# Kernel tuning notes

Hardware: AMD Instinct MI355X
Metric: run time of the kernel (lower is better)

Reference implementation:

```python
import jax, jax.numpy as jnp
import numpy as np

B, L, H = 2, 512, 128

def setup_inputs() -> dict:
    key = jax.random.key(0)
    k1, k2, k3, _ = jax.random.split(key, 4)
    x = jax.random.normal(k1, (B, L, H), jnp.float32)
    y = jax.random.normal(k2, (B, L, H), jnp.float32)
    W_weight = jax.random.normal(k3, (H, 3 * H), jnp.float32) / np.sqrt(3 * H).astype(np.float32)
    W_bias = jnp.zeros((H,), jnp.float32)
    return {"x": x, "y": y, "W_weight": W_weight, "W_bias": W_bias}

def _span_max_context(x):
    """context[b,i,j,h] = max_{k=min(i,j)..max(i,j)} x[b,k,h], shape [B,L,L,H].
    Equivalent to the torch loop of diagonal running-max + symmetric scatter."""
    Bb, Ll, Hh = x.shape
    neg = jnp.full((Bb, 1, Hh), -jnp.inf, x.dtype)
    x_pad = jnp.concatenate([x, neg], axis=1)              # [B,L+1,H]
    d = jnp.arange(Ll)[:, None]                            # diagonal offset
    j = jnp.arange(Ll)[None, :]                            # start position
    shift_idx = jnp.minimum(d + j, Ll)                     # [L,L]; L -> -inf pad
    X2 = x_pad[:, shift_idx, :]                            # X2[b,d,j] = x[b,j+d]
    D = jax.lax.cummax(X2, axis=1)                         # D[b,d,j] = max_{k=j..j+d} x[b,k]
    i = jnp.arange(Ll)[:, None]
    jj = jnp.arange(Ll)[None, :]
    off = jnp.abs(i - jj)                                  # |i-j|
    lo = jnp.minimum(i, jj)                                # min(i,j)
    return D[:, off, lo, :]                                # [B,L,L,H]

def reference(x, y, W_weight, W_bias):
    Hh = x.shape[-1]
    ctx = _span_max_context(x)
    # Split W over the concat [x_i, y_j, context_ij] to avoid a [B,L,L,3H] intermediate.
    Wx, Wy, Wc = W_weight[:, :Hh], W_weight[:, Hh:2 * Hh], W_weight[:, 2 * Hh:]
    t = (jnp.einsum('blh,gh->blg', x, Wx)[:, :, None, :]
         + jnp.einsum('blh,gh->blg', y, Wy)[:, None, :, :]
         + jnp.einsum('bijh,gh->bijg', ctx, Wc)
         + W_bias)
    return jax.nn.gelu(t, approximate=False)               # [B,L,L,H]
```

## Files before the change

kernel.cpp:

```cpp
#include <hip/hip_runtime.h>
#include <hip/hip_bf16.h>

#define LL 512
#define HH 128
#define NBATCH 2
#define NT 32
#define NPAIR (NT*(NT+1)/2)

typedef float f32x4 __attribute__((ext_vector_type(4)));
typedef short s16x8 __attribute__((ext_vector_type(8)));
typedef short s16x4 __attribute__((ext_vector_type(4)));

__device__ __forceinline__ unsigned short f2bfu(float f){
  __hip_bfloat16 h = __float2bfloat16(f);
  return __builtin_bit_cast(unsigned short, h);
}
__device__ __forceinline__ short f2bf(float f){
  __hip_bfloat16 h = __float2bfloat16(f);
  return __builtin_bit_cast(short, h);
}
__device__ __forceinline__ f32x4 max4v(f32x4 a, f32x4 b){
  f32x4 r; r[0]=fmaxf(a[0],b[0]); r[1]=fmaxf(a[1],b[1]);
  r[2]=fmaxf(a[2],b[2]); r[3]=fmaxf(a[3],b[3]); return r;
}
__device__ __forceinline__ float gelu_f(float v){
  float inner = v * fmaf(0.044715f, v*v, 1.0f);
  float e = __expf(1.5957691216f * inner);
  float s = __fdividef(1.0f, e + 1.0f);
  return fmaf(-v, s, v);
}
__device__ __forceinline__ f32x4 gelu4(f32x4 v){
  f32x4 r;
  #pragma unroll
  for (int i=0;i<4;++i) r[i] = gelu_f(v[i]);
  return r;
}

__global__ void prep_kernel(const float* __restrict__ x, const float* __restrict__ y,
                            const float* __restrict__ W, const float* __restrict__ bias,
                            float* __restrict__ t1, float* __restrict__ t2){
  int l = blockIdx.x, b = blockIdx.y;
  __shared__ float xs[HH], ys[HH];
  int tid = threadIdx.x;
  size_t base = ((size_t)b*LL + l)*HH;
  xs[tid] = x[base + tid];
  ys[tid] = y[base + tid];
  __syncthreads();
  const float4* wr1 = (const float4*)(W + (size_t)tid*384);
  const float4* wr2 = (const float4*)(W + (size_t)tid*384 + 128);
  const float4* xs4 = (const float4*)xs;
  const float4* ys4 = (const float4*)ys;
  float s1 = 0.f, s2 = 0.f;
  #pragma unroll
  for (int q=0;q<32;++q){
    float4 a = xs4[q], w = wr1[q];
    s1 = fmaf(a.x,w.x, fmaf(a.y,w.y, fmaf(a.z,w.z, fmaf(a.w,w.w, s1))));
    float4 c = ys4[q], w2 = wr2[q];
    s2 = fmaf(c.x,w2.x, fmaf(c.y,w2.y, fmaf(c.z,w2.z, fmaf(c.w,w2.w, s2))));
  }
  t1[base + tid] = s1 + bias[tid];
  t2[base + tid] = s2;
}

__global__ void misc_kernel(const float* __restrict__ x, const float* __restrict__ W,
                            float* __restrict__ bmax, short* __restrict__ Wcb){
  int blk = blockIdx.x, tid = threadIdx.x;
  if (blk < NBATCH*NT){
    int b = blk >> 5, t = blk & 31;
    float m = -INFINITY;
    #pragma unroll
    for (int r=0;r<16;++r) m = fmaxf(m, x[((size_t)b*LL + t*16 + r)*HH + tid]);
    bmax[(size_t)blk*HH + tid] = m;
  } else {
    int g = blk - NBATCH*NT;
    Wcb[g*HH + tid] = f2bf(W[(size_t)g*384 + 256 + tid]);
  }
}

__global__ __launch_bounds__(512, 4) void ctx_kernel(
    const float* __restrict__ x, const float* __restrict__ t1,
    const float* __restrict__ t2, const float* __restrict__ bmax,
    const short* __restrict__ Wcb, float* __restrict__ out)
{
  __shared__ unsigned short sfxS[16][HH];
  __shared__ unsigned short pfxS[16][HH];
  __shared__ float gmaxS[HH];
  __shared__ unsigned short Atile[256*HH];

  const int tid = threadIdx.x;
  const int b = blockIdx.y;
  int ti = 0, tj;
  { int rem = blockIdx.x;
    while (rem >= NT - ti){ rem -= NT - ti; ++ti; }
    tj = ti + rem; }

  if (ti != tj && tid < 3*HH) {
    int role = tid >> 7;
    int h = tid & (HH-1);
    if (role == 0){
      const float* xp = x + ((size_t)b*LL + ti*16)*HH + h;
      float v[16];
      #pragma unroll
      for (int r=0;r<16;++r) v[r] = xp[(size_t)r*HH];
      float run = -INFINITY;
      #pragma unroll
      for (int r=15;r>=0;--r){ run = fmaxf(run, v[r]); sfxS[r][h] = f2bfu(run); }
    } else if (role == 1){
      const float* xp = x + ((size_t)b*LL + tj*16)*HH + h;
      float v[16];
      #pragma unroll
      for (int r=0;r<16;++r) v[r] = xp[(size_t)r*HH];
      float run = -INFINITY;
      #pragma unroll
      for (int r=0;r<16;++r){ run = fmaxf(run, v[r]); pfxS[r][h] = f2bfu(run); }
    } else {
      float g = -INFINITY;
      for (int t = ti+1; t < tj; ++t)
        g = fmaxf(g, bmax[((size_t)b*NT + t)*HH + h]);
      gmaxS[h] = g;
    }
  }
  __syncthreads();

  {
    const int grp = tid >> 5;
    const int hq  = (tid & 31) * 4;
    auto storeA = [&](int p, f32x4 v){
      int e = p*HH + (hq ^ ((p&7)<<3));
      s16x4 sv = { f2bf(v[0]), f2bf(v[1]), f2bf(v[2]), f2bf(v[3]) };
      *(s16x4*)&Atile[e] = sv;
    };
    auto unpk4 = [&](const unsigned short* pp)->f32x4{
      uint2 u = *(const uint2*)pp;
      f32x4 r;
      r[0] = __uint_as_float(u.x << 16);
      r[1] = __uint_as_float(u.x & 0xFFFF0000u);
      r[2] = __uint_as_float(u.y << 16);
      r[3] = __uint_as_float(u.y & 0xFFFF0000u);
      return r;
    };
    if (ti != tj){
      f32x4 fx = *(const f32x4*)&gmaxS[hq];
      fx = max4v(fx, unpk4(&sfxS[grp][hq]));
      #pragma unroll
      for (int q=0;q<16;++q){
        f32x4 v = max4v(fx, unpk4(&pfxS[q][hq]));
        storeA(grp*16 + q, v);
      }
    } else {
      const float* xbase = x + ((size_t)b*LL + ti*16)*HH + hq;
      f32x4 base = *(const f32x4*)(xbase + (size_t)grp*HH);
      storeA(grp*16 + grp, base);
      f32x4 cur = base;
      for (int q=grp+1;q<16;++q){
        cur = max4v(cur, *(const f32x4*)(xbase + (size_t)q*HH));
        storeA(grp*16 + q, cur);
      }
      cur = base;
      for (int q=grp-1;q>=0;--q){
        cur = max4v(cur, *(const f32x4*)(xbase + (size_t)q*HH));
        storeA(grp*16 + q, cur);
      }
    }
  }
  __syncthreads();

  const int w   = tid >> 6;
  const int l   = tid & 63;
  const int l16 = l & 15, lhi = l >> 4;

  s16x8 wcf[4];
  #pragma unroll
  for (int kb=0;kb<4;++kb)
    wcf[kb] = *(const s16x8*)(Wcb + (size_t)(w*16 + l16)*HH + kb*32 + lhi*8);

  const int g0 = w*16 + lhi*4;
  const int swz = (l16 & 7) << 3;
  const int qrow = tj*16 + l16;
  const size_t t_qoff = ((size_t)b*LL + qrow)*HH + g0;
  const bool offd = (ti != tj);

  #pragma unroll
  for (int pt=0; pt<16; ++pt){
    const int p = pt*16 + l16;
    f32x4 acc = (f32x4){0.f,0.f,0.f,0.f};
    #pragma unroll
    for (int kb=0;kb<4;++kb){
      int hh2 = (kb*32 + lhi*8) ^ swz;
      s16x8 bf8 = *(const s16x8*)&Atile[p*HH + hh2];
      acc = __builtin_amdgcn_mfma_f32_16x16x32_bf16(wcf[kb], bf8, acc, 0, 0, 0);
    }
    const int irow = ti*16 + pt;
    const size_t t_ioff = ((size_t)b*LL + irow)*HH + g0;
    f32x4 t1i = *(const f32x4*)(t1 + t_ioff);
    f32x4 t2j = *(const f32x4*)(t2 + t_qoff);
    f32x4 o1 = gelu4(acc + t1i + t2j);
    *(f32x4*)(out + ((size_t)(b*LL + irow)*LL + qrow)*HH + g0) = o1;
    if (offd){
      f32x4 t1j = *(const f32x4*)(t1 + t_qoff);
      f32x4 t2i = *(const f32x4*)(t2 + t_ioff);
      f32x4 o2 = gelu4(acc + t1j + t2i);
      *(f32x4*)(out + ((size_t)(b*LL + qrow)*LL + irow)*HH + g0) = o2;
    }
  }
}

extern "C" void kernel_launch(void* const* d_in, const int* in_sizes, int n_in,
                              void* d_out, int out_size, void* d_ws, size_t ws_size,
                              hipStream_t stream) {
  const float* x    = (const float*)d_in[0];
  const float* y    = (const float*)d_in[1];
  const float* W    = (const float*)d_in[2];
  const float* bias = (const float*)d_in[3];
  float* out = (float*)d_out;

  float* t1 = (float*)d_ws;
  float* t2 = t1 + (size_t)NBATCH*LL*HH;
  float* bmax = t2 + (size_t)NBATCH*LL*HH;
  short* Wcb = (short*)(bmax + (size_t)NBATCH*NT*HH);

  prep_kernel<<<dim3(LL, NBATCH), HH, 0, stream>>>(x, y, W, bias, t1, t2);
  misc_kernel<<<NBATCH*NT + HH, HH, 0, stream>>>(x, W, bmax, Wcb);
  ctx_kernel<<<dim3(NPAIR, NBATCH), 512, 0, stream>>>(x, t1, t2, bmax, Wcb, out);
}
```

Measured before the change: 98.88 us.

## Build context operand in registers and sparse-table diagonal tiles, merge prep kernels

Folds the misc kernel into the prep kernel, so there is one fewer launch. The off-diagonal path no longer materializes a 64KB LDS A-tile. It folds the global max into the prefix values held in registers, then forms each MFMA operand by taking a packed bf16 max against swizzled suffix rows, which cuts LDS use and raises occupancy. Diagonal tiles now build a log-step sparse table in LDS instead of serial per-thread scans, and the global-max reduction is split over two thread groups. The risks are extra ALU work on packed bf16 and a difference in rounding: prefix and suffix are each rounded to bf16 before the max.

```diff
diff --git a/kernel.cpp b/kernel.cpp
--- a/kernel.cpp
+++ b/kernel.cpp
@@ -5,23 +5,28 @@
 #define HH 128
 #define NBATCH 2
 #define NT 32
-#define NPAIR (NT*(NT+1)/2)
+#define NOFF (NT*(NT-1)/2)
 
 typedef float f32x4 __attribute__((ext_vector_type(4)));
 typedef short s16x8 __attribute__((ext_vector_type(8)));
-typedef short s16x4 __attribute__((ext_vector_type(4)));
+typedef unsigned int u32x4 __attribute__((ext_vector_type(4)));
 
 __device__ __forceinline__ unsigned short f2bfu(float f){
   __hip_bfloat16 h = __float2bfloat16(f);
   return __builtin_bit_cast(unsigned short, h);
 }
-__device__ __forceinline__ short f2bf(float f){
-  __hip_bfloat16 h = __float2bfloat16(f);
-  return __builtin_bit_cast(short, h);
-}
-__device__ __forceinline__ f32x4 max4v(f32x4 a, f32x4 b){
-  f32x4 r; r[0]=fmaxf(a[0],b[0]); r[1]=fmaxf(a[1],b[1]);
-  r[2]=fmaxf(a[2],b[2]); r[3]=fmaxf(a[3],b[3]); return r;
+__device__ __forceinline__ unsigned int bmax2(unsigned int a, unsigned int b){
+  float lo = fmaxf(__uint_as_float(a << 16), __uint_as_float(b << 16));
+  float hi = fmaxf(__uint_as_float(a & 0xFFFF0000u), __uint_as_float(b & 0xFFFF0000u));
+  return __float_as_uint(hi) | (__float_as_uint(lo) >> 16);
+}
+__device__ __forceinline__ unsigned int fold3(unsigned int p, float gl, float gh,
+                                              float g2l, float g2h){
+  float lo = fmaxf(fmaxf(__uint_as_float(p << 16), gl), g2l);
+  float hi = fmaxf(fmaxf(__uint_as_float(p & 0xFFFF0000u), gh), g2h);
+  unsigned int lor = (__float_as_uint(lo) + 0x8000u) >> 16;
+  unsigned int hir = (__float_as_uint(hi) + 0x8000u) & 0xFFFF0000u;
+  return hir | lor;
 }
 __device__ __forceinline__ float gelu_f(float v){
   float inner = v * fmaf(0.044715f, v*v, 1.0f);
@@ -38,42 +43,40 @@
 
 __global__ void prep_kernel(const float* __restrict__ x, const float* __restrict__ y,
                             const float* __restrict__ W, const float* __restrict__ bias,
-                            float* __restrict__ t1, float* __restrict__ t2){
-  int l = blockIdx.x, b = blockIdx.y;
-  __shared__ float xs[HH], ys[HH];
-  int tid = threadIdx.x;
-  size_t base = ((size_t)b*LL + l)*HH;
-  xs[tid] = x[base + tid];
-  ys[tid] = y[base + tid];
-  __syncthreads();
-  const float4* wr1 = (const float4*)(W + (size_t)tid*384);
-  const float4* wr2 = (const float4*)(W + (size_t)tid*384 + 128);
-  const float4* xs4 = (const float4*)xs;
-  const float4* ys4 = (const float4*)ys;
-  float s1 = 0.f, s2 = 0.f;
-  #pragma unroll
-  for (int q=0;q<32;++q){
-    float4 a = xs4[q], w = wr1[q];
-    s1 = fmaf(a.x,w.x, fmaf(a.y,w.y, fmaf(a.z,w.z, fmaf(a.w,w.w, s1))));
-    float4 c = ys4[q], w2 = wr2[q];
-    s2 = fmaf(c.x,w2.x, fmaf(c.y,w2.y, fmaf(c.z,w2.z, fmaf(c.w,w2.w, s2))));
-  }
-  t1[base + tid] = s1 + bias[tid];
-  t2[base + tid] = s2;
-}
-
-__global__ void misc_kernel(const float* __restrict__ x, const float* __restrict__ W,
+                            float* __restrict__ t1, float* __restrict__ t2,
                             float* __restrict__ bmax, short* __restrict__ Wcb){
   int blk = blockIdx.x, tid = threadIdx.x;
-  if (blk < NBATCH*NT){
-    int b = blk >> 5, t = blk & 31;
+  if (blk < NBATCH*LL){
+    int b = blk >> 9, l = blk & (LL-1);
+    __shared__ float xs[HH], ys[HH];
+    size_t base = ((size_t)b*LL + l)*HH;
+    xs[tid] = x[base + tid];
+    ys[tid] = y[base + tid];
+    __syncthreads();
+    const float4* wr1 = (const float4*)(W + (size_t)tid*384);
+    const float4* wr2 = (const float4*)(W + (size_t)tid*384 + 128);
+    const float4* xs4 = (const float4*)xs;
+    const float4* ys4 = (const float4*)ys;
+    float s1 = 0.f, s2 = 0.f;
+    #pragma unroll
+    for (int q=0;q<32;++q){
+      float4 a = xs4[q], w = wr1[q];
+      s1 = fmaf(a.x,w.x, fmaf(a.y,w.y, fmaf(a.z,w.z, fmaf(a.w,w.w, s1))));
+      float4 c = ys4[q], w2 = wr2[q];
+      s2 = fmaf(c.x,w2.x, fmaf(c.y,w2.y, fmaf(c.z,w2.z, fmaf(c.w,w2.w, s2))));
+    }
+    t1[base + tid] = s1 + bias[tid];
+    t2[base + tid] = s2;
+  } else if (blk < NBATCH*LL + NBATCH*NT){
+    int e = blk - NBATCH*LL;
+    int b = e >> 5, t = e & 31;
     float m = -INFINITY;
     #pragma unroll
     for (int r=0;r<16;++r) m = fmaxf(m, x[((size_t)b*LL + t*16 + r)*HH + tid]);
-    bmax[(size_t)blk*HH + tid] = m;
+    bmax[(size_t)e*HH + tid] = m;
   } else {
-    int g = blk - NBATCH*NT;
-    Wcb[g*HH + tid] = f2bf(W[(size_t)g*384 + 256 + tid]);
+    int g = blk - (NBATCH*LL + NBATCH*NT);
+    Wcb[g*HH + tid] = (short)f2bfu(W[(size_t)g*384 + 256 + tid]);
   }
 }
 
@@ -82,125 +85,161 @@
     const float* __restrict__ t2, const float* __restrict__ bmax,
     const short* __restrict__ Wcb, float* __restrict__ out)
 {
-  __shared__ unsigned short sfxS[16][HH];
-  __shared__ unsigned short pfxS[16][HH];
-  __shared__ float gmaxS[HH];
-  __shared__ unsigned short Atile[256*HH];
-
+  __shared__ __align__(16) unsigned int shbuf[5*16*64];
   const int tid = threadIdx.x;
   const int b = blockIdx.y;
-  int ti = 0, tj;
-  { int rem = blockIdx.x;
-    while (rem >= NT - ti){ rem -= NT - ti; ++ti; }
-    tj = ti + rem; }
-
-  if (ti != tj && tid < 3*HH) {
-    int role = tid >> 7;
-    int h = tid & (HH-1);
-    if (role == 0){
-      const float* xp = x + ((size_t)b*LL + ti*16)*HH + h;
-      float v[16];
-      #pragma unroll
-      for (int r=0;r<16;++r) v[r] = xp[(size_t)r*HH];
-      float run = -INFINITY;
-      #pragma unroll
-      for (int r=15;r>=0;--r){ run = fmaxf(run, v[r]); sfxS[r][h] = f2bfu(run); }
-    } else if (role == 1){
-      const float* xp = x + ((size_t)b*LL + tj*16)*HH + h;
-      float v[16];
-      #pragma unroll
-      for (int r=0;r<16;++r) v[r] = xp[(size_t)r*HH];
-      float run = -INFINITY;
-      #pragma unroll
-      for (int r=0;r<16;++r){ run = fmaxf(run, v[r]); pfxS[r][h] = f2bfu(run); }
-    } else {
-      float g = -INFINITY;
-      for (int t = ti+1; t < tj; ++t)
-        g = fmaxf(g, bmax[((size_t)b*NT + t)*HH + h]);
-      gmaxS[h] = g;
-    }
-  }
-  __syncthreads();
-
-  {
-    const int grp = tid >> 5;
-    const int hq  = (tid & 31) * 4;
-    auto storeA = [&](int p, f32x4 v){
-      int e = p*HH + (hq ^ ((p&7)<<3));
-      s16x4 sv = { f2bf(v[0]), f2bf(v[1]), f2bf(v[2]), f2bf(v[3]) };
-      *(s16x4*)&Atile[e] = sv;
-    };
-    auto unpk4 = [&](const unsigned short* pp)->f32x4{
-      uint2 u = *(const uint2*)pp;
-      f32x4 r;
-      r[0] = __uint_as_float(u.x << 16);
-      r[1] = __uint_as_float(u.x & 0xFFFF0000u);
-      r[2] = __uint_as_float(u.y << 16);
-      r[3] = __uint_as_float(u.y & 0xFFFF0000u);
-      return r;
-    };
-    if (ti != tj){
-      f32x4 fx = *(const f32x4*)&gmaxS[hq];
-      fx = max4v(fx, unpk4(&sfxS[grp][hq]));
-      #pragma unroll
-      for (int q=0;q<16;++q){
-        f32x4 v = max4v(fx, unpk4(&pfxS[q][hq]));
-        storeA(grp*16 + q, v);
-      }
-    } else {
-      const float* xbase = x + ((size_t)b*LL + ti*16)*HH + hq;
-      f32x4 base = *(const f32x4*)(xbase + (size_t)grp*HH);
-      storeA(grp*16 + grp, base);
-      f32x4 cur = base;
-      for (int q=grp+1;q<16;++q){
-        cur = max4v(cur, *(const f32x4*)(xbase + (size_t)q*HH));
-        storeA(grp*16 + q, cur);
-      }
-      cur = base;
-      for (int q=grp-1;q>=0;--q){
-        cur = max4v(cur, *(const f32x4*)(xbase + (size_t)q*HH));
-        storeA(grp*16 + q, cur);
-      }
-    }
-  }
-  __syncthreads();
-
-  const int w   = tid >> 6;
-  const int l   = tid & 63;
-  const int l16 = l & 15, lhi = l >> 4;
+  const int w = tid >> 6, l = tid & 63, l16 = l & 15, lhi = l >> 4;
+  const int g0 = w*16 + lhi*4;
 
   s16x8 wcf[4];
   #pragma unroll
   for (int kb=0;kb<4;++kb)
     wcf[kb] = *(const s16x8*)(Wcb + (size_t)(w*16 + l16)*HH + kb*32 + lhi*8);
 
-  const int g0 = w*16 + lhi*4;
-  const int swz = (l16 & 7) << 3;
-  const int qrow = tj*16 + l16;
-  const size_t t_qoff = ((size_t)b*LL + qrow)*HH + g0;
-  const bool offd = (ti != tj);
-
-  #pragma unroll
-  for (int pt=0; pt<16; ++pt){
-    const int p = pt*16 + l16;
-    f32x4 acc = (f32x4){0.f,0.f,0.f,0.f};
+  if (blockIdx.x < NOFF) {
+    int ti = 0, tj;
+    { int rem = blockIdx.x;
+      while (rem >= NT-1-ti){ rem -= NT-1-ti; ++ti; }
+      tj = ti + 1 + rem; }
+
+    unsigned short* sfxU = (unsigned short*)shbuf;
+    unsigned short* pfxU = (unsigned short*)(shbuf + 1024);
+    float* gmaxS = (float*)(shbuf + 2048);
+
+    {
+      int role = tid >> 7, h = tid & 127;
+      if (role == 0){
+        const float* xp = x + ((size_t)b*LL + ti*16)*HH + h;
+        float v[16];
+        #pragma unroll
+        for (int r=0;r<16;++r) v[r] = xp[(size_t)r*HH];
+        float run = -INFINITY;
+        #pragma unroll
+        for (int r=15;r>=0;--r){ run = fmaxf(run, v[r]);
+          sfxU[r*HH + (h ^ ((r&7)<<3))] = f2bfu(run); }
+      } else if (role == 1){
+        const float* xp = x + ((size_t)b*LL + tj*16)*HH + h;
+        float v[16];
+        #pragma unroll
+        for (int r=0;r<16;++r) v[r] = xp[(size_t)r*HH];
+        float run = -INFINITY;
+        #pragma unroll
+        for (int r=0;r<16;++r){ run = fmaxf(run, v[r]);
+          pfxU[r*HH + (h ^ ((r&7)<<3))] = f2bfu(run); }
+      } else {
+        int half = role - 2;
+        float g = -INFINITY;
+        for (int t = ti+1+half; t < tj; t += 2)
+          g = fmaxf(g, bmax[((size_t)b*NT + t)*HH + h]);
+        gmaxS[half*HH + h] = g;
+      }
+    }
+    __syncthreads();
+
+    unsigned int pfxg[16];
+    const unsigned int* pfxW = shbuf + 1024;
     #pragma unroll
     for (int kb=0;kb<4;++kb){
-      int hh2 = (kb*32 + lhi*8) ^ swz;
-      s16x8 bf8 = *(const s16x8*)&Atile[p*HH + hh2];
-      acc = __builtin_amdgcn_mfma_f32_16x16x32_bf16(wcf[kb], bf8, acc, 0, 0, 0);
-    }
-    const int irow = ti*16 + pt;
-    const size_t t_ioff = ((size_t)b*LL + irow)*HH + g0;
-    f32x4 t1i = *(const f32x4*)(t1 + t_ioff);
-    f32x4 t2j = *(const f32x4*)(t2 + t_qoff);
-    f32x4 o1 = gelu4(acc + t1i + t2j);
-    *(f32x4*)(out + ((size_t)(b*LL + irow)*LL + qrow)*HH + g0) = o1;
-    if (offd){
-      f32x4 t1j = *(const f32x4*)(t1 + t_qoff);
-      f32x4 t2i = *(const f32x4*)(t2 + t_ioff);
-      f32x4 o2 = gelu4(acc + t1j + t2i);
-      *(f32x4*)(out + ((size_t)(b*LL + qrow)*LL + irow)*HH + g0) = o2;
+      int h0 = kb*32 + lhi*8;
+      int wd0 = (h0 >> 1) ^ ((l16&7)<<2);
+      u32x4 u = *(const u32x4*)&pfxW[l16*64 + wd0];
+      float4 ga = *(const float4*)&gmaxS[h0];
+      float4 gb = *(const float4*)&gmaxS[h0+4];
+      float4 gc = *(const float4*)&gmaxS[HH + h0];
+      float4 gd = *(const float4*)&gmaxS[HH + h0+4];
+      pfxg[kb*4+0] = fold3(u[0], ga.x, ga.y, gc.x, gc.y);
+      pfxg[kb*4+1] = fold3(u[1], ga.z, ga.w, gc.z, gc.w);
+      pfxg[kb*4+2] = fold3(u[2], gb.x, gb.y, gd.x, gd.y);
+      pfxg[kb*4+3] = fold3(u[3], gb.z, gb.w, gd.z, gd.w);
+    }
+
+    const size_t qoff = ((size_t)b*LL + tj*16 + l16)*HH + g0;
+    f32x4 t1j = *(const f32x4*)(t1 + qoff);
+    f32x4 t2j = *(const f32x4*)(t2 + qoff);
+    const float* t1ip = t1 + ((size_t)b*LL + ti*16)*HH + g0;
+    const float* t2ip = t2 + ((size_t)b*LL + ti*16)*HH + g0;
+    float* o1base = out + (((size_t)(b*LL + ti*16))*LL + tj*16 + l16)*HH + g0;
+    float* o2base = out + (((size_t)(b*LL + tj*16 + l16))*LL + ti*16)*HH + g0;
+    const unsigned int* sfxW = shbuf;
+
+    #pragma unroll
+    for (int pt=0; pt<16; ++pt){
+      f32x4 acc = (f32x4){0.f,0.f,0.f,0.f};
+      #pragma unroll
+      for (int kb=0;kb<4;++kb){
+        int wd0 = ((kb*32 + lhi*8) >> 1) ^ ((pt&7)<<2);
+        u32x4 s = *(const u32x4*)&sfxW[pt*64 + wd0];
+        unsigned int f0 = bmax2(s[0], pfxg[kb*4+0]);
+        unsigned int f1 = bmax2(s[1], pfxg[kb*4+1]);
+        unsigned int f2 = bmax2(s[2], pfxg[kb*4+2]);
+        unsigned int f3 = bmax2(s[3], pfxg[kb*4+3]);
+        u32x4 fr = (u32x4){f0,f1,f2,f3};
+        acc = __builtin_amdgcn_mfma_f32_16x16x32_bf16(wcf[kb],
+                __builtin_bit_cast(s16x8, fr), acc, 0, 0, 0);
+      }
+      f32x4 t1i = *(const f32x4*)(t1ip + (size_t)pt*HH);
+      f32x4 t2i = *(const f32x4*)(t2ip + (size_t)pt*HH);
+      *(f32x4*)(o1base + (size_t)pt*LL*HH) = gelu4(acc + t1i + t2j);
+      *(f32x4*)(o2base + (size_t)pt*HH)    = gelu4(acc + t1j + t2i);
+    }
+  } else {
+    const int td = blockIdx.x - NOFF;
+    #pragma unroll
+    for (int it=0; it<2; ++it){
+      int e = tid*2 + it;
+      int r = e >> 6, wd = e & 63;
+      float2 a = *(const float2*)(x + ((size_t)b*LL + td*16 + r)*HH + wd*2);
+      unsigned int u = ((__float_as_uint(a.y) + 0x8000u) & 0xFFFF0000u)
+                     | ((__float_as_uint(a.x) + 0x8000u) >> 16);
+      shbuf[(0*16 + r)*64 + (wd ^ ((r&7)<<2))] = u;
+    }
+    __syncthreads();
+    #pragma unroll
+    for (int k=1;k<5;++k){
+      int step = 1 << (k-1);
+      unsigned int res[2]; int dst[2];
+      #pragma unroll
+      for (int it=0; it<2; ++it){
+        int e = tid*2 + it;
+        int r = e >> 6, wd = e & 63;
+        int r2 = min(r + step, 15);
+        unsigned int a = shbuf[((k-1)*16 + r )*64 + (wd ^ ((r &7)<<2))];
+        unsigned int c = shbuf[((k-1)*16 + r2)*64 + (wd ^ ((r2&7)<<2))];
+        res[it] = bmax2(a, c);
+        dst[it] = (k*16 + r)*64 + (wd ^ ((r&7)<<2));
+      }
+      shbuf[dst[0]] = res[0];
+      shbuf[dst[1]] = res[1];
+      __syncthreads();
+    }
+
+    const size_t qoff = ((size_t)b*LL + td*16 + l16)*HH + g0;
+    f32x4 t2j = *(const f32x4*)(t2 + qoff);
+    const float* t1ip = t1 + ((size_t)b*LL + td*16)*HH + g0;
+    float* obase = out + (((size_t)(b*LL + td*16))*LL + td*16 + l16)*HH + g0;
+
+    #pragma unroll
+    for (int pt=0; pt<16; ++pt){
+      int a  = min(pt, l16), bb = max(pt, l16);
+      int len = bb - a + 1;
+      int k = 31 - __clz(len);
+      int r2 = bb + 1 - (1 << k);
+      f32x4 acc = (f32x4){0.f,0.f,0.f,0.f};
+      #pragma unroll
+      for (int kb=0;kb<4;++kb){
+        int wd0 = (kb*32 + lhi*8) >> 1;
+        u32x4 ua = *(const u32x4*)&shbuf[(k*16 + a )*64 + ((wd0) ^ ((a &7)<<2))];
+        u32x4 ub = *(const u32x4*)&shbuf[(k*16 + r2)*64 + ((wd0) ^ ((r2&7)<<2))];
+        unsigned int f0 = bmax2(ua[0], ub[0]);
+        unsigned int f1 = bmax2(ua[1], ub[1]);
+        unsigned int f2 = bmax2(ua[2], ub[2]);
+        unsigned int f3 = bmax2(ua[3], ub[3]);
+        u32x4 fr = (u32x4){f0,f1,f2,f3};
+        acc = __builtin_amdgcn_mfma_f32_16x16x32_bf16(wcf[kb],
+                __builtin_bit_cast(s16x8, fr), acc, 0, 0, 0);
+      }
+      f32x4 t1i = *(const f32x4*)(t1ip + (size_t)pt*HH);
+      *(f32x4*)(obase + (size_t)pt*LL*HH) = gelu4(acc + t1i + t2j);
     }
   }
 }
@@ -219,7 +258,6 @@
   float* bmax = t2 + (size_t)NBATCH*LL*HH;
   short* Wcb = (short*)(bmax + (size_t)NBATCH*NT*HH);
 
-  prep_kernel<<<dim3(LL, NBATCH), HH, 0, stream>>>(x, y, W, bias, t1, t2);
-  misc_kernel<<<NBATCH*NT + HH, HH, 0, stream>>>(x, W, bmax, Wcb);
-  ctx_kernel<<<dim3(NPAIR, NBATCH), 512, 0, stream>>>(x, t1, t2, bmax, Wcb, out);
-}
+  prep_kernel<<<NBATCH*LL + NBATCH*NT + HH, HH, 0, stream>>>(x, y, W, bias, t1, t2, bmax, Wcb);
+  ctx_kernel<<<dim3(NOFF + NT, NBATCH), 512, 0, stream>>>(x, t1, t2, bmax, Wcb, out);
+}
```

Result: slower. 109.6 us (+10.8%).
